# Kernel optimization log

Measured on AMD Instinct MI355X. Metric: run time of the kernel, lower is better.

## Reference

```python
import jax, jax.numpy as jnp
import numpy as np

NUM_HEADS = 16


def _apply_rope(x, freqs):
    # x: (H, L, C), freqs: (L, C//2); computed in fp32, cast back to x.dtype
    xf = x.astype(jnp.float32)
    x1, x2 = jnp.split(xf, 2, axis=-1)
    f = freqs.astype(jnp.float32)[None]  # (1, L, C//2)
    cos, sin = jnp.cos(f), jnp.sin(f)
    out = jnp.concatenate((x1 * cos - x2 * sin, x1 * sin + x2 * cos), axis=-1)
    return out.astype(x.dtype)


def setup_inputs() -> dict:
    key = jax.random.key(0)
    k0, k1, k2, k3 = jax.random.split(key, 4)
    S, D, H = 4096, 1280, NUM_HEADS
    hd = D // H
    hidden_states = jax.random.normal(k0, (S, D), dtype=jnp.float32)
    cu_seqlens = jnp.array([0, 1024, 2048, 3072, 4096], dtype=jnp.int32)
    rotary_pos_emb = jax.random.normal(k1, (S, hd // 2), dtype=jnp.float32)
    scale = 1.0 / np.sqrt(D)
    w_qkv = (jax.random.normal(k2, (D, 3 * D), dtype=jnp.float32) * scale)
    b_qkv = jnp.zeros((3 * D,), dtype=jnp.float32)
    w_proj = (jax.random.normal(k3, (D, D), dtype=jnp.float32) * scale)
    b_proj = jnp.zeros((D,), dtype=jnp.float32)
    return {
        "hidden_states": hidden_states,
        "cu_seqlens": cu_seqlens,
        "rotary_pos_emb": rotary_pos_emb,
        "w_qkv": w_qkv,
        "b_qkv": b_qkv,
        "w_proj": w_proj,
        "b_proj": b_proj,
    }


def reference(hidden_states, cu_seqlens, rotary_pos_emb, w_qkv, b_qkv, w_proj, b_proj):
    S, D = hidden_states.shape
    H = NUM_HEADS
    hd = D // H
    qkv = hidden_states @ w_qkv + b_qkv            # (S, 3D)
    qkv = qkv.reshape(S, 3, H, hd).transpose(1, 2, 0, 3)  # (3, H, S, hd)
    q, k, v = qkv[0], qkv[1], qkv[2]
    q = _apply_rope(q, rotary_pos_emb)
    k = _apply_rope(k, rotary_pos_emb)
    # block-diagonal (per-segment) attention, equivalent to the per-segment loop
    seg = jnp.searchsorted(cu_seqlens, jnp.arange(S), side="right") - 1  # (S,)
    mask = seg[:, None] == seg[None, :]            # (S, S)
    scores = jnp.einsum("hqd,hkd->hqk", q, k) / np.sqrt(hd)
    scores = jnp.where(mask[None], scores, -jnp.inf)
    attn = jax.nn.softmax(scores.astype(jnp.float32), axis=-1).astype(q.dtype)
    out = jnp.einsum("hqk,hkd->qhd", attn, v).reshape(S, D)
    return out @ w_proj + b_proj
```

## Files before the change

### kernel.cpp

```cpp
#include <hip/hip_runtime.h>
#include <hip/hip_bf16.h>
#include <cstdint>

typedef __bf16 bf16x8 __attribute__((ext_vector_type(8)));
typedef __bf16 bf16x4 __attribute__((ext_vector_type(4)));
typedef short short4_ __attribute__((ext_vector_type(4)));
typedef float f32x4 __attribute__((ext_vector_type(4)));

#define SLEN 4096
#define DMODEL 1280
#define NHEADS 16
#define HD 80
#define HDP 96
#define KROW 104
#define VTILE_ELEMS 3328
#define VTILE_LDS 3584

#define GLD_LDS16(g, l)                                                        \
  __builtin_amdgcn_global_load_lds(                                            \
      (const __attribute__((address_space(1))) void*)(g),                      \
      (__attribute__((address_space(3))) void*)(l), 16, 0, 0)

#define WAIT_VMCNT(n) __builtin_amdgcn_s_waitcnt((n & 0xF) | 0x70 | 0xF00 | ((n >> 4) << 14))

__global__ __launch_bounds__(256) void cvt_f32_bf16(const float* __restrict__ in,
                                                    __bf16* __restrict__ out, int n4) {
  int i = blockIdx.x * 256 + threadIdx.x;
  if (i < n4) {
    float4 v = ((const float4*)in)[i];
    bf16x4 o = { (__bf16)v.x, (__bf16)v.y, (__bf16)v.z, (__bf16)v.w };
    ((bf16x4*)out)[i] = o;
  }
}

__global__ __launch_bounds__(256) void transpose_cvt(const float* __restrict__ in,
                                                     __bf16* __restrict__ out,
                                                     int K, int N) {
  __shared__ float tile[32][33];
  int n0 = blockIdx.x * 32, k0 = blockIdx.y * 32;
  int x = threadIdx.x & 31, y = threadIdx.x >> 5;
  for (int i = 0; i < 32; i += 8)
    tile[y + i][x] = in[(size_t)(k0 + y + i) * N + n0 + x];
  __syncthreads();
  for (int i = 0; i < 32; i += 8)
    out[(size_t)(n0 + y + i) * K + k0 + x] = (__bf16)tile[x][y + i];
}

template <int WMW>
__global__ __launch_bounds__(WMW * 2 * 64) void gemm_bt(const __bf16* __restrict__ A,
                                                        const __bf16* __restrict__ Bt,
                                                        const float* __restrict__ bias,
                                                        void* __restrict__ C,
                                                        int M, int N, int K, int store_bf16) {
  constexpr int BM = WMW * 64;
  constexpr int NW = WMW * 2;
  constexpr int BI = 8 / NW;
  constexpr int PW = 2 + BI;
  constexpr int ASZ = BM * 32, BSZ = 128 * 32;

  __shared__ __attribute__((aligned(16))) __bf16 As[3][ASZ];
  __shared__ __attribute__((aligned(16))) __bf16 Bs[3][BSZ];

  const int t = threadIdx.x;
  const int lane = t & 63, wave = t >> 6;
  const int quad = lane >> 4, l15 = lane & 15;
  const int wm = (wave & (WMW - 1)) * 64, wn = (wave / WMW) * 64;
  const int bm = blockIdx.x * BM, bn = blockIdx.y * 128;

  const int rs = lane >> 2, cs = (lane & 3) * 8;
  const __bf16* AgQ[2];
  const __bf16* BgQ[BI];
  int aLds[2], bLds[BI];
#pragma unroll
  for (int q = 0; q < 2; ++q) {
    int row = (wave * 2 + q) * 16;
    AgQ[q] = A + (size_t)(bm + row + rs) * K + cs;
    aLds[q] = row * 32;
  }
#pragma unroll
  for (int q = 0; q < BI; ++q) {
    int row = (wave * BI + q) * 16;
    BgQ[q] = Bt + (size_t)(bn + row + rs) * K + cs;
    bLds[q] = row * 32;
  }

  f32x4 acc[4][4] = {};
  const int niter = K >> 5;

#pragma unroll
  for (int s = 0; s < 2; ++s) {
#pragma unroll
    for (int q = 0; q < 2; ++q) GLD_LDS16(AgQ[q] + s * 32, &As[s][aLds[q]]);
#pragma unroll
    for (int q = 0; q < BI; ++q) GLD_LDS16(BgQ[q] + s * 32, &Bs[s][bLds[q]]);
  }

  int cmp = 0, stg = 2;
  for (int it = 0; it < niter; ++it) {
    const int kk = (it + 2 < niter ? it + 2 : niter - 1) * 32;
#pragma unroll
    for (int q = 0; q < 2; ++q) GLD_LDS16(AgQ[q] + kk, &As[stg][aLds[q]]);
#pragma unroll
    for (int q = 0; q < BI; ++q) GLD_LDS16(BgQ[q] + kk, &Bs[stg][bLds[q]]);
    asm volatile("" ::: "memory");
    WAIT_VMCNT(2 * PW);
    __builtin_amdgcn_s_barrier();
    asm volatile("" ::: "memory");

    bf16x8 af[4], bfr[4];
#pragma unroll
    for (int i = 0; i < 4; ++i)
      af[i] = *(const bf16x8*)&As[cmp][(wm + i * 16 + l15) * 32 + quad * 8];
#pragma unroll
    for (int j = 0; j < 4; ++j)
      bfr[j] = *(const bf16x8*)&Bs[cmp][(wn + j * 16 + l15) * 32 + quad * 8];
#pragma unroll
    for (int i = 0; i < 4; ++i)
#pragma unroll
      for (int j = 0; j < 4; ++j)
        acc[i][j] = __builtin_amdgcn_mfma_f32_16x16x32_bf16(af[i], bfr[j], acc[i][j], 0, 0, 0);

    asm volatile("" ::: "memory");
    __builtin_amdgcn_s_barrier();
    asm volatile("" ::: "memory");
    cmp = (cmp == 2) ? 0 : cmp + 1;
    stg = (stg == 2) ? 0 : stg + 1;
  }

  for (int j = 0; j < 4; ++j) {
    int col = bn + wn + j * 16 + l15;
    float bv = bias[col];
    for (int i = 0; i < 4; ++i) {
      int r0 = bm + wm + i * 16 + quad * 4;
      for (int r = 0; r < 4; ++r) {
        float v = acc[i][j][r] + bv;
        if (store_bf16)
          ((__bf16*)C)[(size_t)(r0 + r) * N + col] = (__bf16)v;
        else
          ((float*)C)[(size_t)(r0 + r) * N + col] = v;
      }
    }
  }
}

__global__ __launch_bounds__(256) void rope_pack(const __bf16* __restrict__ qkv,
                                                 const float* __restrict__ freqs,
                                                 __bf16* __restrict__ qp,
                                                 __bf16* __restrict__ kp,
                                                 __bf16* __restrict__ vt) {
  const float QSCALE = 0.11180339887498949f * 1.44269504088896340f;
  int h = blockIdx.y;
  int s0 = blockIdx.x * 64;
  int t = threadIdx.x;
  int sp = t >> 2, l4 = t & 3;
  int s = s0 + sp;
  const __bf16* row = qkv + (size_t)s * 3840 + h * 80;
  __bf16* qo = qp + (size_t)(h * SLEN + s) * HDP;
  __bf16* ko = kp + (size_t)(h * SLEN + s) * KROW;

#pragma unroll
  for (int k = 0; k < 10; ++k) {
    int j = l4 * 10 + k;
    float f = freqs[s * 40 + j];
    float cs = __builtin_cosf(f), sn = __builtin_sinf(f);
    float x1 = (float)row[j], x2 = (float)row[j + 40];
    float y1 = (float)row[1280 + j], y2 = (float)row[1280 + j + 40];
    qo[j]      = (__bf16)((x1 * cs - x2 * sn) * QSCALE);
    qo[j + 40] = (__bf16)((x1 * sn + x2 * cs) * QSCALE);
    ko[j]      = (__bf16)(y1 * cs - y2 * sn);
    ko[j + 40] = (__bf16)(y1 * sn + y2 * cs);
  }
#pragma unroll
  for (int k = 0; k < 4; ++k) {
    int c = 80 + l4 * 4 + k;
    qo[c] = (__bf16)0.f;
    ko[c] = (__bf16)0.f;
  }

  __shared__ float vtile[64][81];
#pragma unroll
  for (int k = 0; k < 20; ++k) {
    int d = l4 * 20 + k;
    vtile[sp][d] = (float)row[2560 + d];
  }
  __syncthreads();
  int key = t & 31, g8 = t >> 5;
  for (int c2 = 0; c2 < 2; ++c2) {
    __bf16* tb = vt + (size_t)(h * (SLEN / 32) + (s0 >> 5) + c2) * VTILE_ELEMS;
#pragma unroll
    for (int k = 0; k < 10; ++k) {
      int d = g8 * 10 + k;
      tb[d * 40 + key] = (__bf16)vtile[c2 * 32 + key][d];
    }
  }
}

__global__ __launch_bounds__(512) void flash_attn(const __bf16* __restrict__ qp,
                                                  const __bf16* __restrict__ kp,
                                                  const __bf16* __restrict__ vt,
                                                  const int* __restrict__ cu, int nseg,
                                                  __bf16* __restrict__ out) {
  const float MEXP = 16.0f;
  int h = blockIdx.y;
  int q0 = blockIdx.x * 128;
  int seg = 0;
  for (int i = 1; i < nseg; ++i)
    if (cu[i] <= q0) seg = i;
  int kstart = cu[seg], kend = cu[seg + 1];

  int t = threadIdx.x;
  int lane = t & 63, wave = t >> 6;
  int quad = lane >> 4, l15 = lane & 15;

  __shared__ __attribute__((aligned(16))) __bf16 Ks[2][64 * KROW];
  __shared__ __attribute__((aligned(16))) __bf16 Vs[2][2 * VTILE_LDS];

  bf16x8 qf[3];
  {
    const __bf16* qptr = qp + (size_t)(h * SLEN + q0 + wave * 16 + l15) * HDP + quad * 8;
    qf[0] = *(const bf16x8*)(qptr);
    qf[1] = *(const bf16x8*)(qptr + 32);
    qf[2] = *(const bf16x8*)(qptr + 64);
  }

  f32x4 o[5] = {};
  float l_p = 0.f;

  const __bf16* gK = kp + (size_t)(h * SLEN + kstart) * KROW + lane * 8;
  const __bf16* gV = vt + (size_t)(h * (SLEN / 32) + (kstart >> 5)) * VTILE_ELEMS + lane * 8;

  const int niter = (kend - kstart) >> 6;

  auto stage = [&](int kn, int buf) {
#pragma unroll
    for (int i0 = 0; i0 < 4; ++i0) {
      int i = wave + i0 * 8;
      int ii = i < 27 ? i : 26;
      if (ii < 13)
        GLD_LDS16(gK + (size_t)kn * (64 * KROW) + ii * 512, &Ks[buf][ii * 512]);
      else if (ii < 20)
        GLD_LDS16(gV + (size_t)kn * (2 * VTILE_ELEMS) + (ii - 13) * 512,
                  &Vs[buf][(ii - 13) * 512]);
      else
        GLD_LDS16(gV + (size_t)kn * (2 * VTILE_ELEMS) + VTILE_ELEMS + (ii - 20) * 512,
                  &Vs[buf][VTILE_LDS + (ii - 20) * 512]);
    }
  };

  stage(0, 0);

  for (int it = 0; it < niter; ++it) {
    const int cur = it & 1, nxt = cur ^ 1;
    const int kn = (it + 1 < niter) ? it + 1 : niter - 1;
    stage(kn, nxt);
    asm volatile("" ::: "memory");
    WAIT_VMCNT(4);
    __builtin_amdgcn_s_barrier();
    asm volatile("" ::: "memory");

    f32x4 sc[4];
#pragma unroll
    for (int nt = 0; nt < 4; ++nt) {
      sc[nt] = f32x4{-MEXP, -MEXP, -MEXP, -MEXP};
#pragma unroll
      for (int c = 0; c < 3; ++c) {
        bf16x8 kf = *(const bf16x8*)&Ks[cur][(nt * 16 + l15) * KROW + quad * 8 + c * 32];
        sc[nt] = __builtin_amdgcn_mfma_f32_16x16x32_bf16(kf, qf[c], sc[nt], 0, 0, 0);
      }
    }

    bf16x4 pf[4];
#pragma unroll
    for (int nt = 0; nt < 4; ++nt)
#pragma unroll
      for (int r = 0; r < 4; ++r) {
        float p = __builtin_amdgcn_exp2f(sc[nt][r]);
        l_p += p;
        pf[nt][r] = (__bf16)p;
      }

#pragma unroll
    for (int kq = 0; kq < 4; ++kq) {
      int vbase = (kq >> 1) * VTILE_LDS + (kq & 1) * 16 + quad * 4;
#pragma unroll
      for (int dt = 0; dt < 5; ++dt) {
        bf16x4 vfr = *(const bf16x4*)&Vs[cur][vbase + (dt * 16 + l15) * 40];
        o[dt] = __builtin_amdgcn_mfma_f32_16x16x16bf16_1k(
            *(short4_*)&vfr, *(short4_*)&pf[kq], o[dt], 0, 0, 0);
      }
    }

    asm volatile("" ::: "memory");
    __builtin_amdgcn_s_barrier();
    asm volatile("" ::: "memory");
  }

  l_p += __shfl_xor(l_p, 16);
  l_p += __shfl_xor(l_p, 32);
  float rinv = 1.0f / l_p;

  int qrow = q0 + wave * 16 + l15;
#pragma unroll
  for (int dt = 0; dt < 5; ++dt) {
    bf16x4 ov;
#pragma unroll
    for (int r = 0; r < 4; ++r)
      ov[r] = (__bf16)(o[dt][r] * rinv);
    *(bf16x4*)&out[(size_t)qrow * DMODEL + h * 80 + dt * 16 + quad * 4] = ov;
  }
}

extern "C" void kernel_launch(void* const* d_in, const int* in_sizes, int n_in,
                              void* d_out, int out_size, void* d_ws, size_t ws_size,
                              hipStream_t stream) {
  const float* hidden = (const float*)d_in[0];
  const int* cu       = (const int*)d_in[1];
  const float* freqs  = (const float*)d_in[2];
  const float* w_qkv  = (const float*)d_in[3];
  const float* b_qkv  = (const float*)d_in[4];
  const float* w_proj = (const float*)d_in[5];
  const float* b_proj = (const float*)d_in[6];
  float* out = (float*)d_out;

  char* ws = (char*)d_ws;
  size_t off = 0;
  auto alloc = [&](size_t bytes) {
    char* p = ws + off;
    off += (bytes + 255) & ~(size_t)255;
    return p;
  };
  __bf16* hid_b  = (__bf16*)alloc((size_t)SLEN * DMODEL * 2);
  __bf16* wqkvT  = (__bf16*)alloc((size_t)3840 * 1280 * 2);
  __bf16* wprojT = (__bf16*)alloc((size_t)1280 * 1280 * 2);
  __bf16* qkvb   = (__bf16*)alloc((size_t)SLEN * 3840 * 2);
  __bf16* qp     = (__bf16*)alloc((size_t)NHEADS * SLEN * HDP * 2);
  __bf16* kp     = (__bf16*)alloc((size_t)NHEADS * SLEN * KROW * 2 + 1024);
  __bf16* vt     = (__bf16*)alloc((size_t)NHEADS * (SLEN / 32) * VTILE_ELEMS * 2 + 1024);
  __bf16* attn   = hid_b;

  cvt_f32_bf16<<<(SLEN * DMODEL / 4 + 255) / 256, 256, 0, stream>>>(hidden, hid_b, SLEN * DMODEL / 4);
  transpose_cvt<<<dim3(3840 / 32, 1280 / 32), 256, 0, stream>>>(w_qkv, wqkvT, 1280, 3840);
  transpose_cvt<<<dim3(1280 / 32, 1280 / 32), 256, 0, stream>>>(w_proj, wprojT, 1280, 1280);
  gemm_bt<4><<<dim3(SLEN / 256, 3840 / 128), 512, 0, stream>>>(hid_b, wqkvT, b_qkv, qkvb,
                                                               SLEN, 3840, 1280, 1);
  rope_pack<<<dim3(SLEN / 64, NHEADS), 256, 0, stream>>>(qkvb, freqs, qp, kp, vt);
  int nseg = in_sizes[1] - 1;
  flash_attn<<<dim3(SLEN / 128, NHEADS), 512, 0, stream>>>(qp, kp, vt, cu, nseg, attn);
  gemm_bt<2><<<dim3(SLEN / 128, DMODEL / 128), 256, 0, stream>>>(attn, wprojT, b_proj, out,
                                                                 SLEN, DMODEL, 1280, 0);
}
```

Measured before the change: 247.6 us.

## Process two query subtiles per wave in flash attention and vectorize rope pack

Flash attention now runs 4 waves per block with each wave owning 32 query rows (two 16-row subtiles), so every K and V fragment read from LDS feeds two MFMAs. This halves LDS traffic per MFMA and is meant to raise MFMA density, at the cost of more registers and fewer waves to hide latency. Staging loads are redistributed across 4 waves (7 per wave). The rope/pack kernel switches to 16-byte vectorized loads and stores, and the V transpose writes bf16x8 chunks.

```diff
diff --git a/kernel.cpp b/kernel.cpp
--- a/kernel.cpp
+++ b/kernel.cpp
@@ -158,44 +158,64 @@
   __bf16* qo = qp + (size_t)(h * SLEN + s) * HDP;
   __bf16* ko = kp + (size_t)(h * SLEN + s) * KROW;
 
-#pragma unroll
-  for (int k = 0; k < 10; ++k) {
-    int j = l4 * 10 + k;
-    float f = freqs[s * 40 + j];
-    float cs = __builtin_cosf(f), sn = __builtin_sinf(f);
-    float x1 = (float)row[j], x2 = (float)row[j + 40];
-    float y1 = (float)row[1280 + j], y2 = (float)row[1280 + j + 40];
-    qo[j]      = (__bf16)((x1 * cs - x2 * sn) * QSCALE);
-    qo[j + 40] = (__bf16)((x1 * sn + x2 * cs) * QSCALE);
-    ko[j]      = (__bf16)(y1 * cs - y2 * sn);
-    ko[j + 40] = (__bf16)(y1 * sn + y2 * cs);
-  }
-#pragma unroll
-  for (int k = 0; k < 4; ++k) {
-    int c = 80 + l4 * 4 + k;
-    qo[c] = (__bf16)0.f;
-    ko[c] = (__bf16)0.f;
-  }
-
   __shared__ float vtile[64][81];
-#pragma unroll
-  for (int k = 0; k < 20; ++k) {
-    int d = l4 * 20 + k;
-    vtile[sp][d] = (float)row[2560 + d];
+
+  for (int c = l4; c < 10; c += 4) {
+    int base = (c < 5) ? c * 8 : (c - 5) * 8;
+    bf16x8 xa = *(const bf16x8*)(row + base);
+    bf16x8 xb = *(const bf16x8*)(row + base + 40);
+    bf16x8 ya = *(const bf16x8*)(row + 1280 + base);
+    bf16x8 yb = *(const bf16x8*)(row + 1280 + base + 40);
+    float4 f0 = *(const float4*)(freqs + s * 40 + base);
+    float4 f1 = *(const float4*)(freqs + s * 40 + base + 4);
+    float fr[8] = {f0.x, f0.y, f0.z, f0.w, f1.x, f1.y, f1.z, f1.w};
+    bf16x8 qv, kv;
+#pragma unroll
+    for (int e = 0; e < 8; ++e) {
+      float cs = __builtin_cosf(fr[e]), sn = __builtin_sinf(fr[e]);
+      float x1 = (float)xa[e], x2 = (float)xb[e];
+      float y1 = (float)ya[e], y2 = (float)yb[e];
+      float qvv, kvv;
+      if (c < 5) { qvv = x1 * cs - x2 * sn; kvv = y1 * cs - y2 * sn; }
+      else       { qvv = x1 * sn + x2 * cs; kvv = y1 * sn + y2 * cs; }
+      qv[e] = (__bf16)(qvv * QSCALE);
+      kv[e] = (__bf16)kvv;
+    }
+    *(bf16x8*)(qo + c * 8) = qv;
+    *(bf16x8*)(ko + c * 8) = kv;
+  }
+  {
+    bf16x8 z = {};
+    if (l4 == 0) *(bf16x8*)(qo + 80) = z;
+    if (l4 == 1) *(bf16x8*)(qo + 88) = z;
+    if (l4 == 2) *(bf16x8*)(ko + 80) = z;
+    if (l4 == 3) *(bf16x8*)(ko + 88) = z;
+  }
+
+  for (int c = l4; c < 10; c += 4) {
+    bf16x8 v = *(const bf16x8*)(row + 2560 + c * 8);
+#pragma unroll
+    for (int e = 0; e < 8; ++e)
+      vtile[sp][c * 8 + e] = (float)v[e];
   }
   __syncthreads();
-  int key = t & 31, g8 = t >> 5;
-  for (int c2 = 0; c2 < 2; ++c2) {
+
+  for (int idx = t; idx < 640; idx += 256) {
+    int c2 = idx >= 320;
+    int rem = idx - (c2 ? 320 : 0);
+    int d = rem >> 2, kc = rem & 3;
     __bf16* tb = vt + (size_t)(h * (SLEN / 32) + (s0 >> 5) + c2) * VTILE_ELEMS;
-#pragma unroll
-    for (int k = 0; k < 10; ++k) {
-      int d = g8 * 10 + k;
-      tb[d * 40 + key] = (__bf16)vtile[c2 * 32 + key][d];
-    }
-  }
-}
-
-__global__ __launch_bounds__(512) void flash_attn(const __bf16* __restrict__ qp,
+    bf16x8 ov;
+#pragma unroll
+    for (int r = 0; r < 4; ++r) {
+      ov[r]     = (__bf16)vtile[c2 * 32 + kc * 4 + r][d];
+      ov[r + 4] = (__bf16)vtile[c2 * 32 + 16 + kc * 4 + r][d];
+    }
+    *(bf16x8*)(tb + d * 40 + kc * 8) = ov;
+  }
+}
+
+__global__ __launch_bounds__(256) void flash_attn(const __bf16* __restrict__ qp,
                                                   const __bf16* __restrict__ kp,
                                                   const __bf16* __restrict__ vt,
                                                   const int* __restrict__ cu, int nseg,
@@ -215,16 +235,17 @@
   __shared__ __attribute__((aligned(16))) __bf16 Ks[2][64 * KROW];
   __shared__ __attribute__((aligned(16))) __bf16 Vs[2][2 * VTILE_LDS];
 
-  bf16x8 qf[3];
-  {
-    const __bf16* qptr = qp + (size_t)(h * SLEN + q0 + wave * 16 + l15) * HDP + quad * 8;
-    qf[0] = *(const bf16x8*)(qptr);
-    qf[1] = *(const bf16x8*)(qptr + 32);
-    qf[2] = *(const bf16x8*)(qptr + 64);
-  }
-
-  f32x4 o[5] = {};
-  float l_p = 0.f;
+  bf16x8 qf[2][3];
+#pragma unroll
+  for (int qs = 0; qs < 2; ++qs) {
+    const __bf16* qptr = qp + (size_t)(h * SLEN + q0 + wave * 32 + qs * 16 + l15) * HDP + quad * 8;
+    qf[qs][0] = *(const bf16x8*)(qptr);
+    qf[qs][1] = *(const bf16x8*)(qptr + 32);
+    qf[qs][2] = *(const bf16x8*)(qptr + 64);
+  }
+
+  f32x4 o[2][5] = {};
+  float l_p[2] = {0.f, 0.f};
 
   const __bf16* gK = kp + (size_t)(h * SLEN + kstart) * KROW + lane * 8;
   const __bf16* gV = vt + (size_t)(h * (SLEN / 32) + (kstart >> 5)) * VTILE_ELEMS + lane * 8;
@@ -232,18 +253,18 @@
   const int niter = (kend - kstart) >> 6;
 
   auto stage = [&](int kn, int buf) {
-#pragma unroll
-    for (int i0 = 0; i0 < 4; ++i0) {
-      int i = wave + i0 * 8;
+    const __bf16* ksrc = gK + (size_t)kn * (64 * KROW);
+    const __bf16* vsrc = gV + (size_t)kn * (2 * VTILE_ELEMS);
+#pragma unroll
+    for (int i0 = 0; i0 < 7; ++i0) {
+      int i = wave * 7 + i0;
       int ii = i < 27 ? i : 26;
       if (ii < 13)
-        GLD_LDS16(gK + (size_t)kn * (64 * KROW) + ii * 512, &Ks[buf][ii * 512]);
+        GLD_LDS16(ksrc + ii * 512, &Ks[buf][ii * 512]);
       else if (ii < 20)
-        GLD_LDS16(gV + (size_t)kn * (2 * VTILE_ELEMS) + (ii - 13) * 512,
-                  &Vs[buf][(ii - 13) * 512]);
+        GLD_LDS16(vsrc + (ii - 13) * 512, &Vs[buf][(ii - 13) * 512]);
       else
-        GLD_LDS16(gV + (size_t)kn * (2 * VTILE_ELEMS) + VTILE_ELEMS + (ii - 20) * 512,
-                  &Vs[buf][VTILE_LDS + (ii - 20) * 512]);
+        GLD_LDS16(vsrc + VTILE_ELEMS + (ii - 20) * 512, &Vs[buf][VTILE_LDS + (ii - 20) * 512]);
     }
   };
 
@@ -254,40 +275,50 @@
     const int kn = (it + 1 < niter) ? it + 1 : niter - 1;
     stage(kn, nxt);
     asm volatile("" ::: "memory");
-    WAIT_VMCNT(4);
+    WAIT_VMCNT(7);
     __builtin_amdgcn_s_barrier();
     asm volatile("" ::: "memory");
 
-    f32x4 sc[4];
+    f32x4 sc[2][4];
 #pragma unroll
     for (int nt = 0; nt < 4; ++nt) {
-      sc[nt] = f32x4{-MEXP, -MEXP, -MEXP, -MEXP};
+      sc[0][nt] = f32x4{-MEXP, -MEXP, -MEXP, -MEXP};
+      sc[1][nt] = sc[0][nt];
 #pragma unroll
       for (int c = 0; c < 3; ++c) {
         bf16x8 kf = *(const bf16x8*)&Ks[cur][(nt * 16 + l15) * KROW + quad * 8 + c * 32];
-        sc[nt] = __builtin_amdgcn_mfma_f32_16x16x32_bf16(kf, qf[c], sc[nt], 0, 0, 0);
+        sc[0][nt] = __builtin_amdgcn_mfma_f32_16x16x32_bf16(kf, qf[0][c], sc[0][nt], 0, 0, 0);
+        sc[1][nt] = __builtin_amdgcn_mfma_f32_16x16x32_bf16(kf, qf[1][c], sc[1][nt], 0, 0, 0);
       }
     }
 
-    bf16x4 pf[4];
-#pragma unroll
-    for (int nt = 0; nt < 4; ++nt)
-#pragma unroll
-      for (int r = 0; r < 4; ++r) {
-        float p = __builtin_amdgcn_exp2f(sc[nt][r]);
-        l_p += p;
-        pf[nt][r] = (__bf16)p;
+    bf16x4 pf[2][4];
+#pragma unroll
+    for (int qs = 0; qs < 2; ++qs)
+#pragma unroll
+      for (int nt = 0; nt < 4; ++nt)
+#pragma unroll
+        for (int r = 0; r < 4; ++r) {
+          float p = __builtin_amdgcn_exp2f(sc[qs][nt][r]);
+          l_p[qs] += p;
+          pf[qs][nt][r] = (__bf16)p;
+        }
+
+#pragma unroll
+    for (int g = 0; g < 2; ++g) {
+#pragma unroll
+      for (int dt = 0; dt < 5; ++dt) {
+        bf16x8 vv = *(const bf16x8*)&Vs[cur][g * VTILE_LDS + (dt * 16 + l15) * 40 + quad * 8];
+        bf16x4 vlo = __builtin_shufflevector(vv, vv, 0, 1, 2, 3);
+        bf16x4 vhi = __builtin_shufflevector(vv, vv, 4, 5, 6, 7);
+#pragma unroll
+        for (int qs = 0; qs < 2; ++qs) {
+          o[qs][dt] = __builtin_amdgcn_mfma_f32_16x16x16bf16_1k(
+              *(short4_*)&vlo, *(short4_*)&pf[qs][g * 2], o[qs][dt], 0, 0, 0);
+          o[qs][dt] = __builtin_amdgcn_mfma_f32_16x16x16bf16_1k(
+              *(short4_*)&vhi, *(short4_*)&pf[qs][g * 2 + 1], o[qs][dt], 0, 0, 0);
+        }
       }
-
-#pragma unroll
-    for (int kq = 0; kq < 4; ++kq) {
-      int vbase = (kq >> 1) * VTILE_LDS + (kq & 1) * 16 + quad * 4;
-#pragma unroll
-      for (int dt = 0; dt < 5; ++dt) {
-        bf16x4 vfr = *(const bf16x4*)&Vs[cur][vbase + (dt * 16 + l15) * 40];
-        o[dt] = __builtin_amdgcn_mfma_f32_16x16x16bf16_1k(
-            *(short4_*)&vfr, *(short4_*)&pf[kq], o[dt], 0, 0, 0);
-      }
     }
 
     asm volatile("" ::: "memory");
@@ -295,18 +326,21 @@
     asm volatile("" ::: "memory");
   }
 
-  l_p += __shfl_xor(l_p, 16);
-  l_p += __shfl_xor(l_p, 32);
-  float rinv = 1.0f / l_p;
-
-  int qrow = q0 + wave * 16 + l15;
-#pragma unroll
-  for (int dt = 0; dt < 5; ++dt) {
-    bf16x4 ov;
-#pragma unroll
-    for (int r = 0; r < 4; ++r)
-      ov[r] = (__bf16)(o[dt][r] * rinv);
-    *(bf16x4*)&out[(size_t)qrow * DMODEL + h * 80 + dt * 16 + quad * 4] = ov;
+#pragma unroll
+  for (int qs = 0; qs < 2; ++qs) {
+    float l = l_p[qs];
+    l += __shfl_xor(l, 16);
+    l += __shfl_xor(l, 32);
+    float rinv = 1.0f / l;
+    int qrow = q0 + wave * 32 + qs * 16 + l15;
+#pragma unroll
+    for (int dt = 0; dt < 5; ++dt) {
+      bf16x4 ov;
+#pragma unroll
+      for (int r = 0; r < 4; ++r)
+        ov[r] = (__bf16)(o[qs][dt][r] * rinv);
+      *(bf16x4*)&out[(size_t)qrow * DMODEL + h * 80 + dt * 16 + quad * 4] = ov;
+    }
   }
 }
 
@@ -345,7 +379,7 @@
                                                                SLEN, 3840, 1280, 1);
   rope_pack<<<dim3(SLEN / 64, NHEADS), 256, 0, stream>>>(qkvb, freqs, qp, kp, vt);
   int nseg = in_sizes[1] - 1;
-  flash_attn<<<dim3(SLEN / 128, NHEADS), 512, 0, stream>>>(qp, kp, vt, cu, nseg, attn);
+  flash_attn<<<dim3(SLEN / 128, NHEADS), 256, 0, stream>>>(qp, kp, vt, cu, nseg, attn);
   gemm_bt<2><<<dim3(SLEN / 128, DMODEL / 128), 256, 0, stream>>>(attn, wprojT, b_proj, out,
                                                                  SLEN, DMODEL, 1280, 0);
 }
```

Result: no change. 244.8 us (-1.2%).
